# Kernel optimization log

Measured on AMD Instinct MI355X. Metric: run time of the kernel, lower is better.

Reference implementation:

```python
import jax, jax.numpy as jnp
import numpy as np

K_HOPS = 3
NUM_GRAPHS = 64
GN_EPS = 1e-5


def setup_inputs() -> dict:
    key = jax.random.key(0)
    ks = jax.random.split(key, 6)
    N, E, F = 50000, 625000, 128
    y = jax.random.normal(ks[0], (N, F), dtype=jnp.float32)
    edge_index = jax.random.randint(ks[1], (2, E), 0, N, dtype=jnp.int64)
    edge_weight = jax.random.uniform(ks[2], (E,), dtype=jnp.float32)
    batch = jnp.sort(jax.random.randint(ks[3], (N,), 0, NUM_GRAPHS, dtype=jnp.int64))
    tag_w = jax.random.normal(ks[4], (K_HOPS + 1, F, F), dtype=jnp.float32) * (1.0 / np.sqrt(F))
    tag_b = jnp.zeros((F,), dtype=jnp.float32)
    gn_weight = jnp.ones((F,), dtype=jnp.float32)
    gn_bias = jnp.zeros((F,), dtype=jnp.float32)
    gn_mean_scale = jnp.ones((F,), dtype=jnp.float32)
    return {"y": y, "edge_index": edge_index, "edge_weight": edge_weight,
            "batch": batch, "tag_w": tag_w, "tag_b": tag_b,
            "gn_weight": gn_weight, "gn_bias": gn_bias, "gn_mean_scale": gn_mean_scale}


def reference(y, edge_index, edge_weight, batch, tag_w, tag_b, gn_weight, gn_bias, gn_mean_scale):
    N = y.shape[0]
    src, dst = edge_index[0], edge_index[1]

    # --- TAGConv: symmetric gcn_norm (no self-loops), K hops ---
    deg = jax.ops.segment_sum(edge_weight, dst, num_segments=N)  # [N]
    dinv = jnp.where(deg > 0, jax.lax.rsqrt(jnp.maximum(deg, 1e-30)), 0.0)
    norm = dinv[src] * edge_weight * dinv[dst]  # [E]

    h = y
    out = h @ tag_w[0]
    for k in range(1, K_HOPS + 1):
        # one hop of message passing: gather from src, scatter-sum at dst
        h = jax.ops.segment_sum(norm[:, None] * h[src], dst, num_segments=N)  # [N,F]
        out = out + h @ tag_w[k]
    out = out + tag_b

    # --- GraphNorm over per-graph segments ---
    cnt = jax.ops.segment_sum(jnp.ones((N,), out.dtype), batch, num_segments=NUM_GRAPHS)
    cnt = jnp.maximum(cnt, 1.0)[:, None]  # [G,1]
    mean = jax.ops.segment_sum(out, batch, num_segments=NUM_GRAPHS) / cnt  # [G,F]
    xc = out - gn_mean_scale * mean[batch]
    var = jax.ops.segment_sum(xc * xc, batch, num_segments=NUM_GRAPHS) / cnt  # [G,F]
    hn = gn_weight * xc * jax.lax.rsqrt(var[batch] + GN_EPS) + gn_bias

    # --- activation; dropout is identity in eval mode; residual ---
    h_act = jax.nn.relu(hn)
    return y + h_act
```

## Files before the change

kernel.cpp:

```cpp
#include <hip/hip_runtime.h>

#define F 128
#define GRAPHS 64
#define GN_EPS 1e-5f
#define PB 256

typedef short short8 __attribute__((ext_vector_type(8)));
typedef float f32x4 __attribute__((ext_vector_type(4)));

__device__ __forceinline__ unsigned short f2b(float f) {
    unsigned u = __float_as_uint(f);
    unsigned r = (u + 0x7fffu + ((u >> 16) & 1u)) >> 16;
    return (unsigned short)r;
}
__device__ __forceinline__ float b2f(unsigned short h) {
    return __uint_as_float(((unsigned)h) << 16);
}

struct MArgs {
    const float* y; const int* ei; const float* ew; const int* batch;
    const float* tw; const float* tb; const float* gnw; const float* gnb; const float* gms;
    float* res;
    float* S1; float* S2; int* gstart; float* dinv; int* offs; int* hist_t; int* bbase;
    uint2* part; unsigned* csr; unsigned short* Wf; unsigned short* hcat; unsigned short* outb;
    int N, E, NB, chunk, fb, gb;
    size_t NF;
};

__global__ __launch_bounds__(256) void k_prep(MArgs a) {
    __shared__ int hist[256];
    const int t0 = 256;
    const int t1 = t0 + a.fb;
    const int t2 = t1 + 256;
    const int t3 = t2 + a.gb;
    int tid = threadIdx.x;
    int task = blockIdx.x;
    if (task < t0) {
        hist[tid] = 0;
        __syncthreads();
        int e0 = task * a.chunk, e1 = min(e0 + a.chunk, a.E);
        for (int e = e0 + tid; e < e1; e += 256)
            atomicAdd(&hist[a.ei[a.E + e] >> 8], 1);
        __syncthreads();
        for (int k = tid; k < a.NB; k += 256)
            a.hist_t[k * PB + task] = hist[k];
    } else if (task < t1) {
        int i = (task - t0) * 256 + tid;
        if (i < a.N * 32) {
            float4 v = ((const float4*)a.y)[i];
            ((ushort4*)a.hcat)[i] = make_ushort4(f2b(v.x), f2b(v.y), f2b(v.z), f2b(v.w));
        }
    } else if (task < t2) {
        int i = (task - t1) * 256 + tid;
        int seg = i >> 14;
        int r = i & 16383;
        int kb = r >> 12;
        int wcc = (r >> 11) & 1;
        int ntt = (r >> 9) & 3;
        int lane = (r >> 3) & 63;
        int j = i & 7;
        int k = kb * 32 + (lane >> 4) * 8 + j;
        int nn = wcc * 64 + ntt * 16 + (lane & 15);
        a.Wf[i] = f2b(a.tw[seg * 16384 + k * 128 + nn]);
    } else if (task < t3) {
        int i = (task - t2) * 256 + tid;
        if (i < a.N) {
            int bb = a.batch[i];
            if (i == 0) {
                for (int g = 0; g <= bb; ++g) a.gstart[g] = 0;
            } else {
                int bp = a.batch[i - 1];
                for (int g = bp + 1; g <= bb; ++g) a.gstart[g] = i;
            }
            if (i == a.N - 1) {
                for (int g = bb + 1; g <= GRAPHS; ++g) a.gstart[g] = a.N;
            }
        }
    } else {
        int z = task - t3;
        float* dst = a.S1 + z * 2048;
        for (int i2 = tid; i2 < 2048; i2 += 256) dst[i2] = 0.f;
    }
}

__global__ __launch_bounds__(256) void k_part(MArgs a) {
    __shared__ int cur[256];
    __shared__ int rs[256];
    int t = threadIdx.x;
    int k = blockIdx.x;
    int total = 0, pref = 0;
    if (t < a.NB) {
        const int4* row = (const int4*)(a.hist_t + t * PB);
        for (int q = 0; q < PB / 4; ++q) {
            int4 v = row[q];
            int c4 = q * 4;
            total += v.x + v.y + v.z + v.w;
            if (c4 + 4 <= k) pref += v.x + v.y + v.z + v.w;
            else {
                if (c4 + 0 < k) pref += v.x;
                if (c4 + 1 < k) pref += v.y;
                if (c4 + 2 < k) pref += v.z;
                if (c4 + 3 < k) pref += v.w;
            }
        }
    }
    rs[t] = (t < a.NB) ? total : 0;
    __syncthreads();
    for (int off = 1; off < 256; off <<= 1) {
        int x = (t >= off) ? rs[t - off] : 0;
        __syncthreads();
        rs[t] += x;
        __syncthreads();
    }
    int rowStart = (t > 0) ? rs[t - 1] : 0;
    cur[t] = rowStart + pref;
    if (k == 0 && t <= a.NB) a.bbase[t] = rowStart;
    __syncthreads();
    int e0 = k * a.chunk, e1 = min(e0 + a.chunk, a.E);
    for (int e = e0 + t; e < e1; e += 256) {
        int dst = a.ei[a.E + e];
        int src = a.ei[e];
        float w = a.ew[e];
        int slot = atomicAdd(&cur[dst >> 8], 1);
        a.part[slot] = make_uint2(((unsigned)dst << 16) | (unsigned)src, __float_as_uint(w));
    }
}

__global__ __launch_bounds__(256) void k_bucket(MArgs a) {
    __shared__ float degf[256];
    __shared__ int cnte[256];
    __shared__ int scn[256];
    __shared__ int cur2[256];
    int t = threadIdx.x;
    int b = blockIdx.x;
    degf[t] = 0.f;
    cnte[t] = 0;
    __syncthreads();
    int s0 = a.bbase[b];
    int s1 = a.bbase[b + 1];
    for (int i = s0 + t; i < s1; i += 256) {
        uint2 pp = a.part[i];
        int dl = (pp.x >> 16) & 255;
        atomicAdd(&degf[dl], __uint_as_float(pp.y));
        atomicAdd(&cnte[dl], 1);
    }
    __syncthreads();
    int v = cnte[t];
    scn[t] = v;
    __syncthreads();
    for (int off = 1; off < 256; off <<= 1) {
        int x = (t >= off) ? scn[t - off] : 0;
        __syncthreads();
        scn[t] += x;
        __syncthreads();
    }
    int node = b * 256 + t;
    int base = s0 + scn[t] - v;
    if (node < a.N) {
        float d = degf[t];
        a.dinv[node] = (d > 0.f) ? rsqrtf(fmaxf(d, 1e-30f)) : 0.f;
        a.offs[node] = base;
    }
    if (b == 0 && t == 0) a.offs[a.N] = a.E;
    cur2[t] = base;
    __syncthreads();
    for (int i = s0 + t; i < s1; i += 256) {
        uint2 pp = a.part[i];
        int dl = (pp.x >> 16) & 255;
        unsigned src = pp.x & 0xffffu;
        int slot = atomicAdd(&cur2[dl], 1);
        a.csr[slot] = (src << 16) | (unsigned)f2b(__uint_as_float(pp.y));
    }
}

template<bool FIX>
__device__ void ph_hop(const MArgs& a, const unsigned short* __restrict__ hin,
                       unsigned short* __restrict__ hout) {
    int lane = threadIdx.x & 63;
    int wv = threadIdx.x >> 6;
    int gq = lane >> 4, fl = lane & 15;
    int node = blockIdx.x * 4 + (threadIdx.x >> 6);
    (void)wv;
    if (node >= a.N) return;
    int e0 = a.offs[node], e1 = a.offs[node + 1];
    float acc[8] = {};
    for (int j = e0; j < e1; j += 16) {
        int base = j + gq * 4;
        unsigned ed0 = (base + 0 < e1) ? a.csr[base + 0] : 0u;
        unsigned ed1 = (base + 1 < e1) ? a.csr[base + 1] : 0u;
        unsigned ed2 = (base + 2 < e1) ? a.csr[base + 2] : 0u;
        unsigned ed3 = (base + 3 < e1) ? a.csr[base + 3] : 0u;
        float w0 = b2f((unsigned short)(ed0 & 0xffffu));
        float w1 = b2f((unsigned short)(ed1 & 0xffffu));
        float w2 = b2f((unsigned short)(ed2 & 0xffffu));
        float w3 = b2f((unsigned short)(ed3 & 0xffffu));
        if (FIX) {
            w0 *= a.dinv[ed0 >> 16];
            w1 *= a.dinv[ed1 >> 16];
            w2 *= a.dinv[ed2 >> 16];
            w3 *= a.dinv[ed3 >> 16];
        }
        short8 h0 = *(const short8*)(hin + (size_t)(ed0 >> 16) * 128 + fl * 8);
        short8 h1 = *(const short8*)(hin + (size_t)(ed1 >> 16) * 128 + fl * 8);
        short8 h2 = *(const short8*)(hin + (size_t)(ed2 >> 16) * 128 + fl * 8);
        short8 h3 = *(const short8*)(hin + (size_t)(ed3 >> 16) * 128 + fl * 8);
        if (FIX && fl < 4) {
            int wi = base + fl;
            if (wi < e1) {
                float wf2 = (fl == 0) ? w0 : (fl == 1) ? w1 : (fl == 2) ? w2 : w3;
                unsigned ede = (fl == 0) ? ed0 : (fl == 1) ? ed1 : (fl == 2) ? ed2 : ed3;
                a.csr[wi] = (ede & 0xffff0000u) | (unsigned)f2b(wf2);
            }
        }
        #pragma unroll
        for (int k = 0; k < 8; ++k) {
            acc[k] += w0 * b2f((unsigned short)h0[k]) + w1 * b2f((unsigned short)h1[k]);
            acc[k] += w2 * b2f((unsigned short)h2[k]) + w3 * b2f((unsigned short)h3[k]);
        }
    }
    #pragma unroll
    for (int k = 0; k < 8; ++k) {
        acc[k] += __shfl_xor(acc[k], 16);
        acc[k] += __shfl_xor(acc[k], 32);
    }
    if (lane < 16) {
        float dd = a.dinv[node];
        short8 o;
        #pragma unroll
        for (int k = 0; k < 8; ++k) o[k] = (short)f2b(acc[k] * dd);
        *(short8*)(hout + (size_t)node * 128 + fl * 8) = o;
    }
}

template<int H>
__global__ __launch_bounds__(256) void k_hop(MArgs a) {
    const unsigned short* hin = a.hcat + (size_t)(H - 1) * a.NF;
    unsigned short* hout = a.hcat + (size_t)H * a.NF;
    if constexpr (H == 1) ph_hop<true>(a, hin, hout);
    else ph_hop<false>(a, hin, hout);
}

__global__ __launch_bounds__(256) void k_gemm(MArgs a) {
    __shared__ unsigned short As[2][4096];
    const unsigned short* __restrict__ hcat = a.hcat;
    const unsigned short* __restrict__ Wf = a.Wf;
    const float* bias = a.tb;
    int M = a.N;
    size_t NF = a.NF;
    int lane = threadIdx.x & 63;
    int wid = threadIdx.x >> 6;
    int wr = wid & 1, wc = wid >> 1;
    int quad = lane >> 4, l15 = lane & 15;
    int row0 = blockIdx.x * 64;
    f32x4 acc[2][4] = {};
    short8 stg[4];
    #pragma unroll
    for (int i = 0; i < 4; ++i) {
        int flat = (wc * 4 + i) * 64 + lane;
        int r = flat >> 4, c = flat & 15;
        stg[i] = *(const short8*)(hcat + (size_t)(row0 + wr * 32 + r) * 128 + c * 8);
    }
    for (int s = 0; s < 4; ++s) {
        __syncthreads();
        #pragma unroll
        for (int i = 0; i < 4; ++i) {
            int flat = (wc * 4 + i) * 64 + lane;
            int r = flat >> 4, c = flat & 15;
            *(short8*)&As[wr][(r * 16 + (c ^ (r & 15))) * 8] = stg[i];
        }
        __syncthreads();
        if (s < 3) {
            const unsigned short* Aseg = hcat + (size_t)(s + 1) * NF;
            #pragma unroll
            for (int i = 0; i < 4; ++i) {
                int flat = (wc * 4 + i) * 64 + lane;
                int r = flat >> 4, c = flat & 15;
                stg[i] = *(const short8*)(Aseg + (size_t)(row0 + wr * 32 + r) * 128 + c * 8);
            }
        }
        #pragma unroll
        for (int kb = 0; kb < 4; ++kb) {
            int swz = ((kb * 4 + quad) ^ l15) * 8;
            short8 a0 = *(short8*)&As[wr][l15 * 128 + swz];
            short8 a1 = *(short8*)&As[wr][(16 + l15) * 128 + swz];
            const unsigned short* bb = Wf + (size_t)(((s * 4 + kb) * 2 + wc) * 4) * 512 + lane * 8;
            short8 b0 = *(const short8*)(bb + 0 * 512);
            short8 b1 = *(const short8*)(bb + 1 * 512);
            short8 b2 = *(const short8*)(bb + 2 * 512);
            short8 b3 = *(const short8*)(bb + 3 * 512);
            acc[0][0] = __builtin_amdgcn_mfma_f32_16x16x32_bf16(a0, b0, acc[0][0], 0, 0, 0);
            acc[0][1] = __builtin_amdgcn_mfma_f32_16x16x32_bf16(a0, b1, acc[0][1], 0, 0, 0);
            acc[0][2] = __builtin_amdgcn_mfma_f32_16x16x32_bf16(a0, b2, acc[0][2], 0, 0, 0);
            acc[0][3] = __builtin_amdgcn_mfma_f32_16x16x32_bf16(a0, b3, acc[0][3], 0, 0, 0);
            acc[1][0] = __builtin_amdgcn_mfma_f32_16x16x32_bf16(a1, b0, acc[1][0], 0, 0, 0);
            acc[1][1] = __builtin_amdgcn_mfma_f32_16x16x32_bf16(a1, b1, acc[1][1], 0, 0, 0);
            acc[1][2] = __builtin_amdgcn_mfma_f32_16x16x32_bf16(a1, b2, acc[1][2], 0, 0, 0);
            acc[1][3] = __builtin_amdgcn_mfma_f32_16x16x32_bf16(a1, b3, acc[1][3], 0, 0, 0);
        }
    }

    float bcol[4];
    #pragma unroll
    for (int nt = 0; nt < 4; ++nt) bcol[nt] = bias[wc * 64 + nt * 16 + l15];
    int rg[2][4];
    #pragma unroll
    for (int mt = 0; mt < 2; ++mt) {
        #pragma unroll
        for (int r = 0; r < 4; ++r) {
            int row = row0 + wr * 32 + mt * 16 + quad * 4 + r;
            rg[mt][r] = (row < M) ? a.batch[row] : -1;
            if (row < M) {
                #pragma unroll
                for (int nt = 0; nt < 4; ++nt) {
                    float vv = acc[mt][nt][r] + bcol[nt];
                    a.outb[(size_t)row * 128 + wc * 64 + nt * 16 + l15] = f2b(vv);
                }
            }
        }
    }
    int glo = a.batch[row0];
    int ghi = a.batch[min(row0 + 63, M - 1)];
    for (int g = glo; g <= ghi; ++g) {
        float s1[4] = {0.f, 0.f, 0.f, 0.f}, s2[4] = {0.f, 0.f, 0.f, 0.f};
        #pragma unroll
        for (int mt = 0; mt < 2; ++mt) {
            #pragma unroll
            for (int r = 0; r < 4; ++r) {
                if (rg[mt][r] == g) {
                    #pragma unroll
                    for (int nt = 0; nt < 4; ++nt) {
                        float vv = acc[mt][nt][r] + bcol[nt];
                        s1[nt] += vv;
                        s2[nt] += vv * vv;
                    }
                }
            }
        }
        #pragma unroll
        for (int nt = 0; nt < 4; ++nt) {
            s1[nt] += __shfl_xor(s1[nt], 16);
            s1[nt] += __shfl_xor(s1[nt], 32);
            s2[nt] += __shfl_xor(s2[nt], 16);
            s2[nt] += __shfl_xor(s2[nt], 32);
        }
        if (quad == 0) {
            #pragma unroll
            for (int nt = 0; nt < 4; ++nt) {
                int col = wc * 64 + nt * 16 + l15;
                atomicAdd(&a.S1[g * 128 + col], s1[nt]);
                atomicAdd(&a.S2[g * 128 + col], s2[nt]);
            }
        }
    }
}

__global__ __launch_bounds__(256) void k_final(MArgs a) {
    int total = a.N * 32;
    const ushort4* yb = (const ushort4*)a.hcat;
    const ushort4* ob = (const ushort4*)a.outb;
    float4* res = (float4*)a.res;
    int idx = blockIdx.x * 256 + threadIdx.x;
    if (idx >= total) return;
    int node = idx >> 5;
    int q = idx & 31;
    int g = a.batch[node];
    float rc = 1.f / fmaxf((float)(a.gstart[g + 1] - a.gstart[g]), 1.f);
    int base = g * 128 + q * 4;
    float4 s1 = *(const float4*)&a.S1[base];
    float4 s2 = *(const float4*)&a.S2[base];
    float4 w  = *(const float4*)&a.gnw[q * 4];
    float4 bb = *(const float4*)&a.gnb[q * 4];
    float4 sc = *(const float4*)&a.gms[q * 4];
    ushort4 yv = yb[idx];
    ushort4 ov = ob[idx];
    float4 r;
    {
        float m = s1.x * rc, e2 = s2.x * rc, s = sc.x;
        float var = e2 - (2.f * s - s * s) * m * m;
        float A = w.x * rsqrtf(var + GN_EPS);
        r.x = b2f(yv.x) + fmaxf(0.f, (b2f(ov.x) - s * m) * A + bb.x);
    }
    {
        float m = s1.y * rc, e2 = s2.y * rc, s = sc.y;
        float var = e2 - (2.f * s - s * s) * m * m;
        float A = w.y * rsqrtf(var + GN_EPS);
        r.y = b2f(yv.y) + fmaxf(0.f, (b2f(ov.y) - s * m) * A + bb.y);
    }
    {
        float m = s1.z * rc, e2 = s2.z * rc, s = sc.z;
        float var = e2 - (2.f * s - s * s) * m * m;
        float A = w.z * rsqrtf(var + GN_EPS);
        r.z = b2f(yv.z) + fmaxf(0.f, (b2f(ov.z) - s * m) * A + bb.z);
    }
    {
        float m = s1.w * rc, e2 = s2.w * rc, s = sc.w;
        float var = e2 - (2.f * s - s * s) * m * m;
        float A = w.w * rsqrtf(var + GN_EPS);
        r.w = b2f(yv.w) + fmaxf(0.f, (b2f(ov.w) - s * m) * A + bb.w);
    }
    res[idx] = r;
}

extern "C" void kernel_launch(void* const* d_in, const int* in_sizes, int n_in,
                              void* d_out, int out_size, void* d_ws, size_t ws_size,
                              hipStream_t stream) {
    const float* y     = (const float*)d_in[0];
    const int*   ei    = (const int*)d_in[1];
    const float* ew    = (const float*)d_in[2];
    const int*   batch = (const int*)d_in[3];
    const float* tag_w = (const float*)d_in[4];
    const float* tag_b = (const float*)d_in[5];
    const float* gnw   = (const float*)d_in[6];
    const float* gnb   = (const float*)d_in[7];
    const float* gms   = (const float*)d_in[8];

    const int N = in_sizes[0] / F;
    const int E = in_sizes[1] / 2;
    const size_t NF = (size_t)N * F;
    const int NB = (N + 255) >> 8;
    const int NH = NB * PB;
    const int chunk = (E + PB - 1) / PB;
    const int fb = (N * 32 + 255) / 256;
    const int gb = (N + 255) / 256;

    char* p = (char*)d_ws;
    float* S1 = (float*)p;       p += (size_t)GRAPHS * F * 4;
    float* S2 = (float*)p;       p += (size_t)GRAPHS * F * 4;
    int*   gstart = (int*)p;     p += 512;
    float* dinv = (float*)p;     p += (size_t)N * 4;
    int*   offs = (int*)p;       p += (size_t)(N + 4) * 4;
    int*   hist_t = (int*)p;     p += (size_t)NH * 4;
    int*   bbase = (int*)p;      p += 1040;
    uint2* part = (uint2*)p;     p += (size_t)E * 8;
    unsigned* csr = (unsigned*)p; p += (size_t)E * 4;
    unsigned short* Wf = (unsigned short*)p; p += 4 * 128 * 128 * 2;
    unsigned short* hcat = (unsigned short*)p; p += NF * 2 * 4;
    unsigned short* outb = (unsigned short*)p; p += NF * 2;
    p += 4096;

    MArgs ha;
    ha.y = y; ha.ei = ei; ha.ew = ew; ha.batch = batch;
    ha.tw = tag_w; ha.tb = tag_b; ha.gnw = gnw; ha.gnb = gnb; ha.gms = gms;
    ha.res = (float*)d_out;
    ha.S1 = S1; ha.S2 = S2; ha.gstart = gstart; ha.dinv = dinv; ha.offs = offs;
    ha.hist_t = hist_t; ha.bbase = bbase; ha.part = part; ha.csr = csr;
    ha.Wf = Wf; ha.hcat = hcat; ha.outb = outb;
    ha.N = N; ha.E = E; ha.NB = NB; ha.chunk = chunk; ha.fb = fb; ha.gb = gb;
    ha.NF = NF;

    k_prep<<<256 + fb + 256 + gb + 8, 256, 0, stream>>>(ha);
    k_part<<<PB, 256, 0, stream>>>(ha);
    k_bucket<<<NB, 256, 0, stream>>>(ha);
    k_hop<1><<<(N + 3) / 4, 256, 0, stream>>>(ha);
    k_hop<2><<<(N + 3) / 4, 256, 0, stream>>>(ha);
    k_hop<3><<<(N + 3) / 4, 256, 0, stream>>>(ha);
    k_gemm<<<(N + 63) / 64, 256, 0, stream>>>(ha);
    k_final<<<(N * 32 + 255) / 256, 256, 0, stream>>>(ha);
}
```

Baseline: 231.0 us.

## Fuse third hop aggregation into the GEMM kernel via shared memory

The third message-passing hop now runs inside the GEMM kernel. Each block gathers neighbor rows for its 64 nodes and writes the aggregated bf16 rows straight into a swizzled LDS tile, which serves as the A operand for the last K-slice. This removes one kernel launch plus the global write and re-read of the hop-3 feature matrix, and shrinks the workspace. In exchange the GEMM blocks do the latency-bound gathers themselves with only 4 waves per 64 nodes, 16 nodes per wave serially, so gather parallelism and occupancy may be lower than in the standalone hop kernel, and LDS use per block doubles.

```diff
diff --git a/kernel.cpp b/kernel.cpp
--- a/kernel.cpp
+++ b/kernel.cpp
@@ -177,10 +177,8 @@
 __device__ void ph_hop(const MArgs& a, const unsigned short* __restrict__ hin,
                        unsigned short* __restrict__ hout) {
     int lane = threadIdx.x & 63;
-    int wv = threadIdx.x >> 6;
     int gq = lane >> 4, fl = lane & 15;
     int node = blockIdx.x * 4 + (threadIdx.x >> 6);
-    (void)wv;
     if (node >= a.N) return;
     int e0 = a.offs[node], e1 = a.offs[node + 1];
     float acc[8] = {};
@@ -240,9 +238,11 @@
     else ph_hop<false>(a, hin, hout);
 }
 
-__global__ __launch_bounds__(256) void k_gemm(MArgs a) {
+__global__ __launch_bounds__(256) void k_hopgemm(MArgs a) {
     __shared__ unsigned short As[2][4096];
+    __shared__ unsigned short As3[2][4096];
     const unsigned short* __restrict__ hcat = a.hcat;
+    const unsigned short* __restrict__ hs2 = a.hcat + 2 * a.NF;
     const unsigned short* __restrict__ Wf = a.Wf;
     const float* bias = a.tb;
     int M = a.N;
@@ -252,6 +252,50 @@
     int wr = wid & 1, wc = wid >> 1;
     int quad = lane >> 4, l15 = lane & 15;
     int row0 = blockIdx.x * 64;
+
+    for (int it = 0; it < 16; ++it) {
+        int ndl = wid * 16 + it;
+        int nd = row0 + ndl;
+        float hacc[8] = {};
+        if (nd < M) {
+            int e0 = a.offs[nd], e1 = a.offs[nd + 1];
+            for (int j = e0; j < e1; j += 16) {
+                int base = j + quad * 4;
+                unsigned ed0 = (base + 0 < e1) ? a.csr[base + 0] : 0u;
+                unsigned ed1 = (base + 1 < e1) ? a.csr[base + 1] : 0u;
+                unsigned ed2 = (base + 2 < e1) ? a.csr[base + 2] : 0u;
+                unsigned ed3 = (base + 3 < e1) ? a.csr[base + 3] : 0u;
+                float w0 = b2f((unsigned short)(ed0 & 0xffffu));
+                float w1 = b2f((unsigned short)(ed1 & 0xffffu));
+                float w2 = b2f((unsigned short)(ed2 & 0xffffu));
+                float w3 = b2f((unsigned short)(ed3 & 0xffffu));
+                short8 h0 = *(const short8*)(hs2 + (size_t)(ed0 >> 16) * 128 + l15 * 8);
+                short8 h1 = *(const short8*)(hs2 + (size_t)(ed1 >> 16) * 128 + l15 * 8);
+                short8 h2 = *(const short8*)(hs2 + (size_t)(ed2 >> 16) * 128 + l15 * 8);
+                short8 h3 = *(const short8*)(hs2 + (size_t)(ed3 >> 16) * 128 + l15 * 8);
+                #pragma unroll
+                for (int k = 0; k < 8; ++k) {
+                    hacc[k] += w0 * b2f((unsigned short)h0[k]) + w1 * b2f((unsigned short)h1[k]);
+                    hacc[k] += w2 * b2f((unsigned short)h2[k]) + w3 * b2f((unsigned short)h3[k]);
+                }
+            }
+        }
+        #pragma unroll
+        for (int k = 0; k < 8; ++k) {
+            hacc[k] += __shfl_xor(hacc[k], 16);
+            hacc[k] += __shfl_xor(hacc[k], 32);
+        }
+        if (lane < 16) {
+            float dd = (nd < M) ? a.dinv[nd] : 0.f;
+            short8 o;
+            #pragma unroll
+            for (int k = 0; k < 8; ++k) o[k] = (short)f2b(hacc[k] * dd);
+            int rr = ndl & 31;
+            *(short8*)&As3[ndl >> 5][(rr * 16 + (l15 ^ (rr & 15))) * 8] = o;
+        }
+    }
+    __syncthreads();
+
     f32x4 acc[2][4] = {};
     short8 stg[4];
     #pragma unroll
@@ -261,28 +305,34 @@
         stg[i] = *(const short8*)(hcat + (size_t)(row0 + wr * 32 + r) * 128 + c * 8);
     }
     for (int s = 0; s < 4; ++s) {
-        __syncthreads();
-        #pragma unroll
-        for (int i = 0; i < 4; ++i) {
-            int flat = (wc * 4 + i) * 64 + lane;
-            int r = flat >> 4, c = flat & 15;
-            *(short8*)&As[wr][(r * 16 + (c ^ (r & 15))) * 8] = stg[i];
-        }
-        __syncthreads();
+        const unsigned short* AsP;
         if (s < 3) {
-            const unsigned short* Aseg = hcat + (size_t)(s + 1) * NF;
+            __syncthreads();
             #pragma unroll
             for (int i = 0; i < 4; ++i) {
                 int flat = (wc * 4 + i) * 64 + lane;
                 int r = flat >> 4, c = flat & 15;
-                stg[i] = *(const short8*)(Aseg + (size_t)(row0 + wr * 32 + r) * 128 + c * 8);
-            }
+                *(short8*)&As[wr][(r * 16 + (c ^ (r & 15))) * 8] = stg[i];
+            }
+            __syncthreads();
+            if (s < 2) {
+                const unsigned short* Aseg = hcat + (size_t)(s + 1) * NF;
+                #pragma unroll
+                for (int i = 0; i < 4; ++i) {
+                    int flat = (wc * 4 + i) * 64 + lane;
+                    int r = flat >> 4, c = flat & 15;
+                    stg[i] = *(const short8*)(Aseg + (size_t)(row0 + wr * 32 + r) * 128 + c * 8);
+                }
+            }
+            AsP = As[wr];
+        } else {
+            AsP = As3[wr];
         }
         #pragma unroll
         for (int kb = 0; kb < 4; ++kb) {
             int swz = ((kb * 4 + quad) ^ l15) * 8;
-            short8 a0 = *(short8*)&As[wr][l15 * 128 + swz];
-            short8 a1 = *(short8*)&As[wr][(16 + l15) * 128 + swz];
+            short8 a0 = *(const short8*)&AsP[l15 * 128 + swz];
+            short8 a1 = *(const short8*)&AsP[(16 + l15) * 128 + swz];
             const unsigned short* bb = Wf + (size_t)(((s * 4 + kb) * 2 + wc) * 4) * 512 + lane * 8;
             short8 b0 = *(const short8*)(bb + 0 * 512);
             short8 b1 = *(const short8*)(bb + 1 * 512);
@@ -434,7 +484,7 @@
     uint2* part = (uint2*)p;     p += (size_t)E * 8;
     unsigned* csr = (unsigned*)p; p += (size_t)E * 4;
     unsigned short* Wf = (unsigned short*)p; p += 4 * 128 * 128 * 2;
-    unsigned short* hcat = (unsigned short*)p; p += NF * 2 * 4;
+    unsigned short* hcat = (unsigned short*)p; p += NF * 2 * 3;
     unsigned short* outb = (unsigned short*)p; p += NF * 2;
     p += 4096;
 
@@ -453,7 +503,6 @@
     k_bucket<<<NB, 256, 0, stream>>>(ha);
     k_hop<1><<<(N + 3) / 4, 256, 0, stream>>>(ha);
     k_hop<2><<<(N + 3) / 4, 256, 0, stream>>>(ha);
-    k_hop<3><<<(N + 3) / 4, 256, 0, stream>>>(ha);
-    k_gemm<<<(N + 63) / 64, 256, 0, stream>>>(ha);
+    k_hopgemm<<<(N + 63) / 64, 256, 0, stream>>>(ha);
     k_final<<<(N * 32 + 255) / 256, 256, 0, stream>>>(ha);
 }
```

New measurement: 256.6 us. 1.11x slower.

## Precompute partition offsets with a two-pass global scan and stage CSR in LDS

Applied to the files above, without the earlier changes.

Replaces the per-block redundant prefix computation in k_part, where each of 256 blocks re-read the whole histogram, with two small scan kernels that compute the exclusive offsets once. k_part then only loads its starting cursors. k_bucket now writes its scattered CSR entries into a shared-memory buffer and copies them out with coalesced stores, falling back to global writes when a bucket overflows the buffer. This adds two kernel launches and 24 KB of LDS per bucket block, which may lower occupancy.

```diff
diff --git a/kernel.cpp b/kernel.cpp
--- a/kernel.cpp
+++ b/kernel.cpp
@@ -4,6 +4,8 @@
 #define GRAPHS 64
 #define GN_EPS 1e-5f
 #define PB 256
+#define SCAN_B 256
+#define CSRBUF 6144
 
 typedef short short8 __attribute__((ext_vector_type(8)));
 typedef float f32x4 __attribute__((ext_vector_type(4)));
@@ -21,7 +23,8 @@
     const float* y; const int* ei; const float* ew; const int* batch;
     const float* tw; const float* tb; const float* gnw; const float* gnb; const float* gms;
     float* res;
-    float* S1; float* S2; int* gstart; float* dinv; int* offs; int* hist_t; int* bbase;
+    float* S1; float* S2; int* gstart; float* dinv; int* offs; int* hist_t; int* ex;
+    int* blockSums; int* bbase;
     uint2* part; unsigned* csr; unsigned short* Wf; unsigned short* hcat; unsigned short* outb;
     int N, E, NB, chunk, fb, gb;
     size_t NF;
@@ -83,38 +86,51 @@
     }
 }
 
+__global__ void k_scanA(MArgs a) {
+    __shared__ int s[SCAN_B];
+    int n = a.NB * PB;
+    int i = blockIdx.x * SCAN_B + threadIdx.x;
+    int v = (i < n) ? a.hist_t[i] : 0;
+    s[threadIdx.x] = v;
+    __syncthreads();
+    for (int off = 1; off < SCAN_B; off <<= 1) {
+        int t = (threadIdx.x >= off) ? s[threadIdx.x - off] : 0;
+        __syncthreads();
+        s[threadIdx.x] += t;
+        __syncthreads();
+    }
+    if (i < n) a.ex[i] = s[threadIdx.x] - v;
+    if (threadIdx.x == SCAN_B - 1) a.blockSums[blockIdx.x] = s[SCAN_B - 1];
+}
+
+__global__ void k_scanB(MArgs a) {
+    __shared__ int s[SCAN_B];
+    int n = a.NB * PB;
+    int nb = (n + SCAN_B - 1) / SCAN_B;
+    int t = threadIdx.x;
+    int v = (t < nb) ? a.blockSums[t] : 0;
+    s[t] = v;
+    __syncthreads();
+    for (int off = 1; off < SCAN_B; off <<= 1) {
+        int x = (t >= off) ? s[t - off] : 0;
+        __syncthreads();
+        s[t] += x;
+        __syncthreads();
+    }
+    int pre = (blockIdx.x == 0) ? 0 : s[blockIdx.x - 1];
+    int i = blockIdx.x * SCAN_B + t;
+    if (i < n) a.ex[i] += pre;
+}
+
 __global__ __launch_bounds__(256) void k_part(MArgs a) {
     __shared__ int cur[256];
-    __shared__ int rs[256];
     int t = threadIdx.x;
     int k = blockIdx.x;
-    int total = 0, pref = 0;
-    if (t < a.NB) {
-        const int4* row = (const int4*)(a.hist_t + t * PB);
-        for (int q = 0; q < PB / 4; ++q) {
-            int4 v = row[q];
-            int c4 = q * 4;
-            total += v.x + v.y + v.z + v.w;
-            if (c4 + 4 <= k) pref += v.x + v.y + v.z + v.w;
-            else {
-                if (c4 + 0 < k) pref += v.x;
-                if (c4 + 1 < k) pref += v.y;
-                if (c4 + 2 < k) pref += v.z;
-                if (c4 + 3 < k) pref += v.w;
-            }
-        }
-    }
-    rs[t] = (t < a.NB) ? total : 0;
-    __syncthreads();
-    for (int off = 1; off < 256; off <<= 1) {
-        int x = (t >= off) ? rs[t - off] : 0;
-        __syncthreads();
-        rs[t] += x;
-        __syncthreads();
-    }
-    int rowStart = (t > 0) ? rs[t - 1] : 0;
-    cur[t] = rowStart + pref;
-    if (k == 0 && t <= a.NB) a.bbase[t] = rowStart;
+    cur[t] = (t < a.NB) ? a.ex[t * PB + k] : 0;
+    if (k == 0) {
+        if (t < a.NB) a.bbase[t] = a.ex[t * PB];
+        if (t == 0) a.bbase[a.NB] = a.E;
+    }
     __syncthreads();
     int e0 = k * a.chunk, e1 = min(e0 + a.chunk, a.E);
     for (int e = e0 + t; e < e1; e += 256) {
@@ -131,6 +147,7 @@
     __shared__ int cnte[256];
     __shared__ int scn[256];
     __shared__ int cur2[256];
+    __shared__ unsigned csrb[CSRBUF];
     int t = threadIdx.x;
     int b = blockIdx.x;
     degf[t] = 0.f;
@@ -169,18 +186,23 @@
         int dl = (pp.x >> 16) & 255;
         unsigned src = pp.x & 0xffffu;
         int slot = atomicAdd(&cur2[dl], 1);
-        a.csr[slot] = (src << 16) | (unsigned)f2b(__uint_as_float(pp.y));
-    }
+        unsigned val = (src << 16) | (unsigned)f2b(__uint_as_float(pp.y));
+        int loc = slot - s0;
+        if (loc < CSRBUF) csrb[loc] = val;
+        else a.csr[slot] = val;
+    }
+    __syncthreads();
+    int len = min(s1 - s0, CSRBUF);
+    for (int i = t; i < len; i += 256)
+        a.csr[s0 + i] = csrb[i];
 }
 
 template<bool FIX>
 __device__ void ph_hop(const MArgs& a, const unsigned short* __restrict__ hin,
                        unsigned short* __restrict__ hout) {
     int lane = threadIdx.x & 63;
-    int wv = threadIdx.x >> 6;
     int gq = lane >> 4, fl = lane & 15;
     int node = blockIdx.x * 4 + (threadIdx.x >> 6);
-    (void)wv;
     if (node >= a.N) return;
     int e0 = a.offs[node], e1 = a.offs[node + 1];
     float acc[8] = {};
@@ -430,6 +452,8 @@
     float* dinv = (float*)p;     p += (size_t)N * 4;
     int*   offs = (int*)p;       p += (size_t)(N + 4) * 4;
     int*   hist_t = (int*)p;     p += (size_t)NH * 4;
+    int*   ex = (int*)p;         p += (size_t)(NH + 4) * 4;
+    int*   blockSums = (int*)p;  p += 4096;
     int*   bbase = (int*)p;      p += 1040;
     uint2* part = (uint2*)p;     p += (size_t)E * 8;
     unsigned* csr = (unsigned*)p; p += (size_t)E * 4;
@@ -443,12 +467,16 @@
     ha.tw = tag_w; ha.tb = tag_b; ha.gnw = gnw; ha.gnb = gnb; ha.gms = gms;
     ha.res = (float*)d_out;
     ha.S1 = S1; ha.S2 = S2; ha.gstart = gstart; ha.dinv = dinv; ha.offs = offs;
-    ha.hist_t = hist_t; ha.bbase = bbase; ha.part = part; ha.csr = csr;
+    ha.hist_t = hist_t; ha.ex = ex; ha.blockSums = blockSums; ha.bbase = bbase;
+    ha.part = part; ha.csr = csr;
     ha.Wf = Wf; ha.hcat = hcat; ha.outb = outb;
     ha.N = N; ha.E = E; ha.NB = NB; ha.chunk = chunk; ha.fb = fb; ha.gb = gb;
     ha.NF = NF;
 
+    const int hsb = (NH + SCAN_B - 1) / SCAN_B;
     k_prep<<<256 + fb + 256 + gb + 8, 256, 0, stream>>>(ha);
+    k_scanA<<<hsb, SCAN_B, 0, stream>>>(ha);
+    k_scanB<<<hsb, SCAN_B, 0, stream>>>(ha);
     k_part<<<PB, 256, 0, stream>>>(ha);
     k_bucket<<<NB, 256, 0, stream>>>(ha);
     k_hop<1><<<(N + 3) / 4, 256, 0, stream>>>(ha);
```

After: 244.9 us. +6.0%, slower.
